# Kernel tuning notes

Measured on AMD Instinct MI355X. Metric: run time of the kernel, lower is better.

Reference implementation:

```python
import jax, jax.numpy as jnp
import numpy as np

N_NODES = 50000
N_EDGES = 500000
D_IN = 128
D_OUT = 128
NUM_GRAPHS = 512


def sage_conv(x, src, dst, W_l, W_r, num_nodes):
    # mean aggregation of source-node features onto target nodes
    msg = x[src]  # [E, D]
    agg = jax.ops.segment_sum(msg, dst, num_segments=num_nodes)
    cnt = jax.ops.segment_sum(jnp.ones((src.shape[0], 1), x.dtype), dst,
                              num_segments=num_nodes)
    agg = agg / jnp.maximum(cnt, 1.0)
    # PyG SAGEConv (bias=False): lin_l(agg) + lin_r(x); torch Linear is x @ W.T
    return agg @ W_l.T + x @ W_r.T


def setup_inputs() -> dict:
    key = jax.random.key(0)
    ks = jax.random.split(key, 7)
    x = jax.random.normal(ks[0], (N_NODES, D_IN), dtype=jnp.float32)
    edge_index = jax.random.randint(ks[1], (2, N_EDGES), 0, N_NODES, dtype=jnp.int64)
    batch = jnp.sort(jax.random.randint(ks[2], (N_NODES,), 0, NUM_GRAPHS, dtype=jnp.int64))
    s = 1.0 / np.sqrt(D_IN)
    W_l1 = jax.random.uniform(ks[3], (D_OUT, D_IN), jnp.float32, -s, s)
    W_r1 = jax.random.uniform(ks[4], (D_OUT, D_IN), jnp.float32, -s, s)
    W_l2 = jax.random.uniform(ks[5], (D_OUT, D_OUT), jnp.float32, -s, s)
    W_r2 = jax.random.uniform(ks[6], (D_OUT, D_OUT), jnp.float32, -s, s)
    return {"x": x, "edge_index": edge_index, "batch": batch,
            "W_l1": W_l1, "W_r1": W_r1, "W_l2": W_l2, "W_r2": W_r2}


def reference(x, edge_index, batch, W_l1, W_r1, W_l2, W_r2):
    src, dst = edge_index[0], edge_index[1]
    # dropout p=0.0 -> identity
    x1 = jax.nn.relu(sage_conv(x, src, dst, W_l1, W_r1, N_NODES))
    x2 = jax.nn.relu(sage_conv(x1, src, dst, W_l2, W_r2, N_NODES))
    xs = jnp.concatenate([x1, x2], axis=-1)  # JumpingKnowledge('cat')
    pooled = jax.ops.segment_max(xs, batch, num_segments=NUM_GRAPHS)
    # guard empty graphs (segment_max yields -inf there)
    return jnp.where(jnp.isfinite(pooled), pooled, 0.0)
```

## Files before the change

### kernel.cpp

```cpp
#include <hip/hip_runtime.h>
#include <hip/hip_bf16.h>

#define N_NODES 50000
#define N_EDGES 500000
#define D 128
#define NUM_GRAPHS 512
#define BM 128
#define NB_NODES 196
#define CVT_BLOCKS 6250

typedef __attribute__((ext_vector_type(8))) short bf16x8;
typedef __attribute__((ext_vector_type(4))) float f32x4;

static __device__ __forceinline__ unsigned short f2b(float f) {
  __hip_bfloat16 h = __float2bfloat16(f);
  return *reinterpret_cast<unsigned short*>(&h);
}
static __device__ __forceinline__ float blo(unsigned int p) {
  return __uint_as_float(p << 16);
}
static __device__ __forceinline__ float bhi(unsigned int p) {
  return __uint_as_float(p & 0xffff0000u);
}


__global__ __launch_bounds__(256) void k_prep(
    const float* __restrict__ x, unsigned short* __restrict__ xb,
    const int* __restrict__ batch, int* __restrict__ gstart,
    int* __restrict__ deg) {
  int b = blockIdx.x;
  if (b < NB_NODES) {
    int i = b * 256 + threadIdx.x;
    if (i < N_NODES) {
      deg[i] = 0;
      int bb = batch[i];
      int prev = (i == 0) ? -1 : batch[i - 1];
      for (int g = prev + 1; g <= bb; ++g) gstart[g] = i;
      if (i == N_NODES - 1)
        for (int g = bb + 1; g <= NUM_GRAPHS; ++g) gstart[g] = N_NODES;
    }
  } else {
    int i = ((b - NB_NODES) * 256 + threadIdx.x) * 4;
    if (i < N_NODES * D) {
      float4 f = *(const float4*)&x[i];
      ushort4 o = make_ushort4(f2b(f.x), f2b(f.y), f2b(f.z), f2b(f.w));
      *(ushort4*)&xb[i] = o;
    }
  }
}


__global__ void k_count(const int* __restrict__ dst, int* __restrict__ deg) {
  int e = blockIdx.x * 256 + threadIdx.x;
  if (e < N_EDGES) atomicAdd(&deg[dst[e]], 1);
}

__global__ void k_scan1(const int* __restrict__ deg, int* __restrict__ bsum) {
  __shared__ int s[256];
  int t = threadIdx.x;
  int i = blockIdx.x * 256 + t;
  s[t] = (i < N_NODES) ? deg[i] : 0;
  __syncthreads();
  for (int off = 128; off > 0; off >>= 1) {
    if (t < off) s[t] += s[t + off];
    __syncthreads();
  }
  if (t == 0) bsum[blockIdx.x] = s[0];
}

__global__ void k_scan2(int* __restrict__ bsum, int nb) {
  __shared__ int s[256];
  int t = threadIdx.x;
  int v = (t < nb) ? bsum[t] : 0;
  s[t] = v;
  __syncthreads();
  for (int off = 1; off < 256; off <<= 1) {
    int add = (t >= off) ? s[t - off] : 0;
    __syncthreads();
    s[t] += add;
    __syncthreads();
  }
  if (t < nb) bsum[t] = s[t] - v;
}

__global__ void k_scan3(const int* __restrict__ deg, const int* __restrict__ bsum,
                        int* __restrict__ rowptr, int* __restrict__ pos) {
  __shared__ int s[256];
  int t = threadIdx.x;
  int i = blockIdx.x * 256 + t;
  int v = (i < N_NODES) ? deg[i] : 0;
  s[t] = v;
  __syncthreads();
  for (int off = 1; off < 256; off <<= 1) {
    int add = (t >= off) ? s[t - off] : 0;
    __syncthreads();
    s[t] += add;
    __syncthreads();
  }
  int excl = s[t] - v + bsum[blockIdx.x];
  if (i < N_NODES) { rowptr[i] = excl; pos[i] = excl; }
  if (i == N_NODES - 1) rowptr[N_NODES] = excl + v;
}

__global__ void k_bucket(const int* __restrict__ src, const int* __restrict__ dst,
                         int* __restrict__ pos, int* __restrict__ esrc) {
  int e = blockIdx.x * 256 + threadIdx.x;
  if (e < N_EDGES) {
    int slot = atomicAdd(&pos[dst[e]], 1);
    esrc[slot] = src[e];
  }
}


__global__ __launch_bounds__(256) void k_agg(
    const unsigned short* __restrict__ xb, const int* __restrict__ rowptr,
    const int* __restrict__ esrc, unsigned short* __restrict__ aggb) {
  int node = (blockIdx.x * 256 + threadIdx.x) >> 6;
  int lane = threadIdx.x & 63;
  if (node >= N_NODES) return;
  int beg = rowptr[node], end = rowptr[node + 1];
  float ax = 0.f, ay = 0.f;
  int e = beg;
  for (; e + 4 <= end; e += 4) {
    unsigned int p0 = *(const unsigned int*)&xb[(size_t)esrc[e] * D + lane * 2];
    unsigned int p1 = *(const unsigned int*)&xb[(size_t)esrc[e + 1] * D + lane * 2];
    unsigned int p2 = *(const unsigned int*)&xb[(size_t)esrc[e + 2] * D + lane * 2];
    unsigned int p3 = *(const unsigned int*)&xb[(size_t)esrc[e + 3] * D + lane * 2];
    ax += blo(p0) + blo(p1) + blo(p2) + blo(p3);
    ay += bhi(p0) + bhi(p1) + bhi(p2) + bhi(p3);
  }
  for (; e < end; ++e) {
    unsigned int p = *(const unsigned int*)&xb[(size_t)esrc[e] * D + lane * 2];
    ax += blo(p);
    ay += bhi(p);
  }
  float inv = 1.f / fmaxf((float)(end - beg), 1.f);
  unsigned int o = (unsigned int)f2b(ax * inv) | ((unsigned int)f2b(ay * inv) << 16);
  *(unsigned int*)&aggb[(size_t)node * D + lane * 2] = o;
}


__global__ __launch_bounds__(512) void k_gemm(
    const unsigned short* Ab, const unsigned short* __restrict__ Xb,
    const float* __restrict__ Wl, const float* __restrict__ Wr,
    unsigned short* Yb) {
  __shared__ unsigned short Wlds[32768];
  const int tid = threadIdx.x;
  const int w = tid >> 6, lane = tid & 63;
  const int lr = lane & 15, lh = lane >> 4;
  const int row0 = blockIdx.x * BM;
  const int row = row0 + w * 16 + lr;

  bf16x8 a[8];
  if (row < N_NODES) {
    const unsigned short* ar = Ab + (size_t)row * D;
    const unsigned short* xr = Xb + (size_t)row * D;
#pragma unroll
    for (int kk = 0; kk < 4; ++kk)
      a[kk] = *(const bf16x8*)(ar + kk * 32 + lh * 8);
#pragma unroll
    for (int kk = 0; kk < 4; ++kk)
      a[4 + kk] = *(const bf16x8*)(xr + kk * 32 + lh * 8);
  } else {
#pragma unroll
    for (int kk = 0; kk < 8; ++kk)
      a[kk] = (bf16x8){0, 0, 0, 0, 0, 0, 0, 0};
  }

  {
    int j = tid >> 2, quarter = tid & 3;
    const float* srcp = (quarter < 2) ? (Wl + j * D + quarter * 64)
                                      : (Wr + j * D + (quarter - 2) * 64);
#pragma unroll
    for (int q = 0; q < 8; ++q) {
      float4 f0 = *(const float4*)(srcp + q * 8);
      float4 f1 = *(const float4*)(srcp + q * 8 + 4);
      bf16x8 wv;
      wv[0] = (short)f2b(f0.x); wv[1] = (short)f2b(f0.y);
      wv[2] = (short)f2b(f0.z); wv[3] = (short)f2b(f0.w);
      wv[4] = (short)f2b(f1.x); wv[5] = (short)f2b(f1.y);
      wv[6] = (short)f2b(f1.z); wv[7] = (short)f2b(f1.w);
      int byteofs = j * 512 + ((quarter * 128 + q * 16) ^ ((j & 7) << 4));
      *(bf16x8*)((char*)Wlds + byteofs) = wv;
    }
  }
  __syncthreads();

  f32x4 acc[8];
#pragma unroll
  for (int jt = 0; jt < 8; ++jt) acc[jt] = (f32x4){0.f, 0.f, 0.f, 0.f};

#pragma unroll
  for (int jt = 0; jt < 8; ++jt) {
    int jj = jt * 16 + lr;
    const char* wbase = (const char*)Wlds + jj * 512;
    int sw = (jj & 7) << 4;
#pragma unroll
    for (int kk = 0; kk < 8; ++kk) {
      bf16x8 b = *(const bf16x8*)(wbase + ((kk * 64 + lh * 16) ^ sw));
      acc[jt] = __builtin_amdgcn_mfma_f32_16x16x32_bf16(a[kk], b, acc[jt], 0, 0, 0);
    }
  }

  __syncthreads();
#pragma unroll
  for (int jt = 0; jt < 8; ++jt) {
#pragma unroll
    for (int r = 0; r < 4; ++r) {
      int rl = w * 16 + lh * 4 + r;
      int col = jt * 16 + lr;
      float v = acc[jt][r];
      v = v > 0.f ? v : 0.f;
      int byteofs = rl * 256 + ((col * 2) ^ ((rl & 7) << 4));
      *(unsigned short*)((char*)Wlds + byteofs) = f2b(v);
    }
  }
  __syncthreads();
  {
    int rl = tid >> 2, c0 = (tid & 3) * 64;
    int grow = row0 + rl;
    if (grow < N_NODES) {
#pragma unroll
      for (int cc = 0; cc < 4; ++cc) {
        int byteofs = rl * 256 + ((c0 + cc * 16) ^ ((rl & 7) << 4));
        bf16x8 v = *(const bf16x8*)((char*)Wlds + byteofs);
        *(bf16x8*)&Yb[(size_t)grow * D + (c0 + cc * 16) / 2] = v;
      }
    }
  }
}


__global__ __launch_bounds__(256) void k_pool(
    const unsigned short* __restrict__ x1b, const unsigned short* __restrict__ x2b,
    const int* __restrict__ gstart, float* __restrict__ out) {
  int g = blockIdx.x, tid = threadIdx.x;
  int beg = gstart[g], end = gstart[g + 1];
  const unsigned short* base = (tid < D) ? (x1b + tid) : (x2b + (tid - D));
  float m = 0.f;
  int r = beg;
  for (; r + 4 <= end; r += 4) {
    float a = __uint_as_float((unsigned int)base[(size_t)r * D] << 16);
    float b = __uint_as_float((unsigned int)base[(size_t)(r + 1) * D] << 16);
    float c = __uint_as_float((unsigned int)base[(size_t)(r + 2) * D] << 16);
    float d = __uint_as_float((unsigned int)base[(size_t)(r + 3) * D] << 16);
    m = fmaxf(m, fmaxf(fmaxf(a, b), fmaxf(c, d)));
  }
  for (; r < end; ++r)
    m = fmaxf(m, __uint_as_float((unsigned int)base[(size_t)r * D] << 16));
  out[g * (2 * D) + tid] = m;
}


extern "C" void kernel_launch(void* const* d_in, const int* in_sizes, int n_in,
                              void* d_out, int out_size, void* d_ws, size_t ws_size,
                              hipStream_t stream) {
  const float* x = (const float*)d_in[0];
  const int* ei = (const int*)d_in[1];
  const int* src = ei;
  const int* dst = ei + N_EDGES;
  const int* batch = (const int*)d_in[2];
  const float* Wl1 = (const float*)d_in[3];
  const float* Wr1 = (const float*)d_in[4];
  const float* Wl2 = (const float*)d_in[5];
  const float* Wr2 = (const float*)d_in[6];
  float* out = (float*)d_out;

  char* ws = (char*)d_ws;
  size_t off = 0;
  auto alloc = [&](size_t bytes) -> void* {
    void* p = ws + off;
    off += (bytes + 511) & ~(size_t)511;
    return p;
  };
  int* deg = (int*)alloc((size_t)N_NODES * 4);
  int* rowptr = (int*)alloc((size_t)(N_NODES + 1) * 4);
  int* pos = (int*)alloc((size_t)N_NODES * 4);
  int* bsum = (int*)alloc(256 * 4);
  int* gstart = (int*)alloc((size_t)(NUM_GRAPHS + 1) * 4);
  int* esrc = (int*)alloc((size_t)N_EDGES * 4);
  unsigned short* xb = (unsigned short*)alloc((size_t)N_NODES * D * 2);
  unsigned short* aggb = (unsigned short*)alloc((size_t)N_NODES * D * 2);
  unsigned short* x1b = (unsigned short*)alloc((size_t)N_NODES * D * 2);
  (void)ws_size; (void)in_sizes; (void)n_in; (void)out_size;

  k_prep<<<NB_NODES + CVT_BLOCKS, 256, 0, stream>>>(x, xb, batch, gstart, deg);

  k_count<<<(N_EDGES + 255) / 256, 256, 0, stream>>>(dst, deg);
  k_scan1<<<NB_NODES, 256, 0, stream>>>(deg, bsum);
  k_scan2<<<1, 256, 0, stream>>>(bsum, NB_NODES);
  k_scan3<<<NB_NODES, 256, 0, stream>>>(deg, bsum, rowptr, pos);
  k_bucket<<<(N_EDGES + 255) / 256, 256, 0, stream>>>(src, dst, pos, esrc);

  int agg_blocks = (N_NODES * 64 + 255) / 256;
  int gemm_blocks = (N_NODES + BM - 1) / BM;

  k_agg<<<agg_blocks, 256, 0, stream>>>(xb, rowptr, esrc, aggb);
  k_gemm<<<gemm_blocks, 512, 0, stream>>>(aggb, xb, Wl1, Wr1, x1b);
  k_agg<<<agg_blocks, 256, 0, stream>>>(x1b, rowptr, esrc, aggb);
  k_gemm<<<gemm_blocks, 512, 0, stream>>>(aggb, x1b, Wl2, Wr2, aggb);
  k_pool<<<NUM_GRAPHS, 256, 0, stream>>>(x1b, aggb, gstart, out);
}
```

Measured before the change: 170.6 us.

## Fuse max-pooling into GEMM epilogue, merge scan kernels into one block

Drops the separate pooling kernel: each GEMM block runs a segmented max over its rows in LDS, grouping by batch id, and issues atomicMax on the output, reading the bf16 bits as unsigned ints. This is valid because the values are non-negative after ReLU. The second GEMM no longer writes x2 to global memory, and the output is zeroed in the prep kernel. The three-kernel prefix scan becomes a single 1024-thread block, and the gstart computation is removed. The cost is extra global atomics and a serial per-column loop in the GEMM epilogue, and the single-block scan has limited parallelism.

```diff
diff --git a/kernel.cpp b/kernel.cpp
--- a/kernel.cpp
+++ b/kernel.cpp
@@ -8,6 +8,9 @@
 #define BM 128
 #define NB_NODES 196
 #define CVT_BLOCKS 6250
+#define OUT_BLOCKS 128
+#define SCAN_T 1024
+#define PER_T 49
 
 typedef __attribute__((ext_vector_type(8))) short bf16x8;
 typedef __attribute__((ext_vector_type(4))) float f32x4;
@@ -26,26 +29,22 @@
 
 __global__ __launch_bounds__(256) void k_prep(
     const float* __restrict__ x, unsigned short* __restrict__ xb,
-    const int* __restrict__ batch, int* __restrict__ gstart,
-    int* __restrict__ deg) {
+    int* __restrict__ deg, float* __restrict__ out) {
   int b = blockIdx.x;
   if (b < NB_NODES) {
     int i = b * 256 + threadIdx.x;
-    if (i < N_NODES) {
-      deg[i] = 0;
-      int bb = batch[i];
-      int prev = (i == 0) ? -1 : batch[i - 1];
-      for (int g = prev + 1; g <= bb; ++g) gstart[g] = i;
-      if (i == N_NODES - 1)
-        for (int g = bb + 1; g <= NUM_GRAPHS; ++g) gstart[g] = N_NODES;
-    }
-  } else {
+    if (i < N_NODES) deg[i] = 0;
+  } else if (b < NB_NODES + CVT_BLOCKS) {
     int i = ((b - NB_NODES) * 256 + threadIdx.x) * 4;
     if (i < N_NODES * D) {
       float4 f = *(const float4*)&x[i];
       ushort4 o = make_ushort4(f2b(f.x), f2b(f.y), f2b(f.z), f2b(f.w));
       *(ushort4*)&xb[i] = o;
     }
+  } else {
+    int i = ((b - NB_NODES - CVT_BLOCKS) * 256 + threadIdx.x) * 4;
+    if (i < NUM_GRAPHS * 2 * D)
+      *(float4*)&out[i] = make_float4(0.f, 0.f, 0.f, 0.f);
   }
 }
 
@@ -55,51 +54,36 @@
   if (e < N_EDGES) atomicAdd(&deg[dst[e]], 1);
 }
 
-__global__ void k_scan1(const int* __restrict__ deg, int* __restrict__ bsum) {
-  __shared__ int s[256];
+__global__ __launch_bounds__(SCAN_T) void k_scan(
+    const int* __restrict__ deg, int* __restrict__ rowptr, int* __restrict__ pos) {
+  __shared__ int ssum[SCAN_T];
   int t = threadIdx.x;
-  int i = blockIdx.x * 256 + t;
-  s[t] = (i < N_NODES) ? deg[i] : 0;
-  __syncthreads();
-  for (int off = 128; off > 0; off >>= 1) {
-    if (t < off) s[t] += s[t + off];
+  int base = t * PER_T;
+  int s = 0;
+#pragma unroll 4
+  for (int i = 0; i < PER_T; ++i) {
+    int idx = base + i;
+    if (idx < N_NODES) s += deg[idx];
+  }
+  ssum[t] = s;
+  __syncthreads();
+  for (int off = 1; off < SCAN_T; off <<= 1) {
+    int add = (t >= off) ? ssum[t - off] : 0;
     __syncthreads();
-  }
-  if (t == 0) bsum[blockIdx.x] = s[0];
-}
-
-__global__ void k_scan2(int* __restrict__ bsum, int nb) {
-  __shared__ int s[256];
-  int t = threadIdx.x;
-  int v = (t < nb) ? bsum[t] : 0;
-  s[t] = v;
-  __syncthreads();
-  for (int off = 1; off < 256; off <<= 1) {
-    int add = (t >= off) ? s[t - off] : 0;
+    ssum[t] += add;
     __syncthreads();
-    s[t] += add;
-    __syncthreads();
-  }
-  if (t < nb) bsum[t] = s[t] - v;
-}
-
-__global__ void k_scan3(const int* __restrict__ deg, const int* __restrict__ bsum,
-                        int* __restrict__ rowptr, int* __restrict__ pos) {
-  __shared__ int s[256];
-  int t = threadIdx.x;
-  int i = blockIdx.x * 256 + t;
-  int v = (i < N_NODES) ? deg[i] : 0;
-  s[t] = v;
-  __syncthreads();
-  for (int off = 1; off < 256; off <<= 1) {
-    int add = (t >= off) ? s[t - off] : 0;
-    __syncthreads();
-    s[t] += add;
-    __syncthreads();
-  }
-  int excl = s[t] - v + bsum[blockIdx.x];
-  if (i < N_NODES) { rowptr[i] = excl; pos[i] = excl; }
-  if (i == N_NODES - 1) rowptr[N_NODES] = excl + v;
+  }
+  int run = ssum[t] - s;
+#pragma unroll 4
+  for (int i = 0; i < PER_T; ++i) {
+    int idx = base + i;
+    if (idx < N_NODES) {
+      rowptr[idx] = run;
+      pos[idx] = run;
+      run += deg[idx];
+    }
+  }
+  if (t == SCAN_T - 1) rowptr[N_NODES] = ssum[SCAN_T - 1];
 }
 
 __global__ void k_bucket(const int* __restrict__ src, const int* __restrict__ dst,
@@ -141,10 +125,11 @@
 
 
 __global__ __launch_bounds__(512) void k_gemm(
-    const unsigned short* Ab, const unsigned short* __restrict__ Xb,
+    const unsigned short* __restrict__ Ab, const unsigned short* __restrict__ Xb,
     const float* __restrict__ Wl, const float* __restrict__ Wr,
-    unsigned short* Yb) {
-  __shared__ unsigned short Wlds[32768];
+    unsigned short* __restrict__ Yb, const int* __restrict__ batch,
+    unsigned int* __restrict__ pool, int col_ofs) {
+  __shared__ unsigned short Wlds[32768 + 256];
   const int tid = threadIdx.x;
   const int w = tid >> 6, lane = tid & 63;
   const int lr = lane & 15, lh = lane >> 4;
@@ -215,8 +200,14 @@
       *(unsigned short*)((char*)Wlds + byteofs) = f2b(v);
     }
   }
-  __syncthreads();
-  {
+  int* sb = (int*)(Wlds + 32768);
+  if (tid < BM) {
+    int grow = row0 + tid;
+    sb[tid] = (grow < N_NODES) ? batch[grow] : -1;
+  }
+  __syncthreads();
+
+  if (Yb != nullptr) {
     int rl = tid >> 2, c0 = (tid & 3) * 64;
     int grow = row0 + rl;
     if (grow < N_NODES) {
@@ -228,27 +219,27 @@
       }
     }
   }
-}
-
-
-__global__ __launch_bounds__(256) void k_pool(
-    const unsigned short* __restrict__ x1b, const unsigned short* __restrict__ x2b,
-    const int* __restrict__ gstart, float* __restrict__ out) {
-  int g = blockIdx.x, tid = threadIdx.x;
-  int beg = gstart[g], end = gstart[g + 1];
-  const unsigned short* base = (tid < D) ? (x1b + tid) : (x2b + (tid - D));
-  float m = 0.f;
-  int r = beg;
-  for (; r + 4 <= end; r += 4) {
-    float a = __uint_as_float((unsigned int)base[(size_t)r * D] << 16);
-    float b = __uint_as_float((unsigned int)base[(size_t)(r + 1) * D] << 16);
-    float c = __uint_as_float((unsigned int)base[(size_t)(r + 2) * D] << 16);
-    float d = __uint_as_float((unsigned int)base[(size_t)(r + 3) * D] << 16);
-    m = fmaxf(m, fmaxf(fmaxf(a, b), fmaxf(c, d)));
-  }
-  for (; r < end; ++r)
-    m = fmaxf(m, __uint_as_float((unsigned int)base[(size_t)r * D] << 16));
-  out[g * (2 * D) + tid] = m;
+
+  if (tid < 256) {
+    int col = tid & 127;
+    int r0 = (tid >> 7) * 64;
+    unsigned short run = 0;
+    int curg = sb[r0];
+    for (int r = r0; r < r0 + 64; ++r) {
+      int g = sb[r];
+      if (g != curg) {
+        if (curg >= 0 && run)
+          atomicMax(&pool[curg * (2 * D) + col_ofs + col], ((unsigned int)run) << 16);
+        curg = g;
+        run = 0;
+      }
+      int byteofs = r * 256 + ((col * 2) ^ ((r & 7) << 4));
+      unsigned short v = *(const unsigned short*)((char*)Wlds + byteofs);
+      run = run > v ? run : v;
+    }
+    if (curg >= 0 && run)
+      atomicMax(&pool[curg * (2 * D) + col_ofs + col], ((unsigned int)run) << 16);
+  }
 }
 
 
@@ -264,7 +255,6 @@
   const float* Wr1 = (const float*)d_in[4];
   const float* Wl2 = (const float*)d_in[5];
   const float* Wr2 = (const float*)d_in[6];
-  float* out = (float*)d_out;
 
   char* ws = (char*)d_ws;
   size_t off = 0;
@@ -276,28 +266,26 @@
   int* deg = (int*)alloc((size_t)N_NODES * 4);
   int* rowptr = (int*)alloc((size_t)(N_NODES + 1) * 4);
   int* pos = (int*)alloc((size_t)N_NODES * 4);
-  int* bsum = (int*)alloc(256 * 4);
-  int* gstart = (int*)alloc((size_t)(NUM_GRAPHS + 1) * 4);
   int* esrc = (int*)alloc((size_t)N_EDGES * 4);
   unsigned short* xb = (unsigned short*)alloc((size_t)N_NODES * D * 2);
   unsigned short* aggb = (unsigned short*)alloc((size_t)N_NODES * D * 2);
   unsigned short* x1b = (unsigned short*)alloc((size_t)N_NODES * D * 2);
   (void)ws_size; (void)in_sizes; (void)n_in; (void)out_size;
 
-  k_prep<<<NB_NODES + CVT_BLOCKS, 256, 0, stream>>>(x, xb, batch, gstart, deg);
+  k_prep<<<NB_NODES + CVT_BLOCKS + OUT_BLOCKS, 256, 0, stream>>>(
+      x, xb, deg, (float*)d_out);
 
   k_count<<<(N_EDGES + 255) / 256, 256, 0, stream>>>(dst, deg);
-  k_scan1<<<NB_NODES, 256, 0, stream>>>(deg, bsum);
-  k_scan2<<<1, 256, 0, stream>>>(bsum, NB_NODES);
-  k_scan3<<<NB_NODES, 256, 0, stream>>>(deg, bsum, rowptr, pos);
+  k_scan<<<1, SCAN_T, 0, stream>>>(deg, rowptr, pos);
   k_bucket<<<(N_EDGES + 255) / 256, 256, 0, stream>>>(src, dst, pos, esrc);
 
   int agg_blocks = (N_NODES * 64 + 255) / 256;
   int gemm_blocks = (N_NODES + BM - 1) / BM;
 
   k_agg<<<agg_blocks, 256, 0, stream>>>(xb, rowptr, esrc, aggb);
-  k_gemm<<<gemm_blocks, 512, 0, stream>>>(aggb, xb, Wl1, Wr1, x1b);
+  k_gemm<<<gemm_blocks, 512, 0, stream>>>(aggb, xb, Wl1, Wr1, x1b, batch,
+                                          (unsigned int*)d_out, 0);
   k_agg<<<agg_blocks, 256, 0, stream>>>(x1b, rowptr, esrc, aggb);
-  k_gemm<<<gemm_blocks, 512, 0, stream>>>(aggb, x1b, Wl2, Wr2, aggb);
-  k_pool<<<NUM_GRAPHS, 256, 0, stream>>>(x1b, aggb, gstart, out);
-}
+  k_gemm<<<gemm_blocks, 512, 0, stream>>>(aggb, x1b, Wl2, Wr2, nullptr, batch,
+                                          (unsigned int*)d_out, D);
+}
```

After: 282.9 us. 1.66x slower.
